# Optimization experiments

Measured on AMD Instinct MI355X. Metric: run time of the kernel, lower is better.

## Reference

```python
import jax, jax.numpy as jnp
import numpy as np

C = 128          # hidden width hard-coded in DirModelToFace
EPS = 1e-5       # BatchNorm1d eps


def sparse_bmm(rows, cols, vals, x, num_rows):
    """Batched sparse @ dense: COO (rows, cols, vals) shared across batch.
    x: [B, K, c] -> [B, num_rows, c]."""
    def one(xb):
        return jax.ops.segment_sum(xb[cols] * vals[:, None], rows, num_segments=num_rows)
    return jax.vmap(one)(x)


def conv1x1_prebn(x, gamma, beta, W, b):
    # GraphConv1x1(batch_norm='pre'): BN (training stats over B*N rows) then Linear
    mean = x.mean((0, 1))
    var = x.var((0, 1))  # biased, as torch BN uses for normalization
    xh = (x - mean) * jax.lax.rsqrt(var + EPS) * gamma + beta
    return xh @ W + b


def dir_block(Di, DiA, v, f, g, be, W, b):
    # DirResNet2 (res_f=False): quaternionic Dirac message passing
    B, N, _ = v.shape
    Fn = f.shape[1]
    msg_v = sparse_bmm(*DiA, f.reshape(B, 4 * Fn, C // 4), 4 * N).reshape(B, N, C)
    x = jax.nn.elu(jnp.concatenate([v, msg_v], axis=-1))
    v_out = v + conv1x1_prebn(x, g[0], be[0], W[0], b[0])
    msg_f = sparse_bmm(*Di, v_out.reshape(B, 4 * N, C // 4), 4 * Fn).reshape(B, Fn, C)
    x = jax.nn.elu(jnp.concatenate([f, msg_f], axis=-1))
    f_out = conv1x1_prebn(x, g[1], be[1], W[1], b[1])  # no residual on f
    return v_out, f_out


def avg_block(mask, v, g, be, W, b):
    # AvgResNet2: masked global average message
    x = v
    for j in range(2):
        x = jax.nn.elu(x)
        x_avg = (mask * x).sum(1, keepdims=True) / mask.sum(1, keepdims=True)
        x = jnp.concatenate([x, jnp.broadcast_to(x_avg, x.shape)], axis=-1)
        x = conv1x1_prebn(x, g[j], be[j], W[j], b[j])
    return x + v


def setup_inputs() -> dict:
    key = jax.random.key(0)
    ks = jax.random.split(key, 10)
    B, N, Fn = 4, 12000, 24000
    nnz = 48 * Fn  # 3 vertices per face x 4x4 quaternion block
    inputs = jax.random.normal(ks[0], (B, N, 3), jnp.float32)
    mask = jnp.ones((B, N, 1), jnp.float32)
    Di_rows = jax.random.randint(ks[1], (nnz,), 0, 4 * Fn, jnp.int32)
    Di_cols = jax.random.randint(ks[2], (nnz,), 0, 4 * N, jnp.int32)
    Di_vals = jax.random.normal(ks[3], (nnz,), jnp.float32) * 0.1
    DiA_rows = jax.random.randint(ks[4], (nnz,), 0, 4 * N, jnp.int32)
    DiA_cols = jax.random.randint(ks[5], (nnz,), 0, 4 * Fn, jnp.int32)
    DiA_vals = jax.random.normal(ks[6], (nnz,), jnp.float32) * 0.1
    W1 = jax.random.normal(ks[7], (3, C), jnp.float32) / np.sqrt(3.0)
    b1 = jnp.zeros((C,), jnp.float32)
    rn_gamma = jnp.ones((16, 2, 2 * C), jnp.float32)
    rn_beta = jnp.zeros((16, 2, 2 * C), jnp.float32)
    rn_W = jax.random.normal(ks[8], (16, 2, 2 * C, C), jnp.float32) / np.sqrt(2.0 * C)
    rn_b = jnp.zeros((16, 2, C), jnp.float32)
    g2 = jnp.ones((C,), jnp.float32)
    be2 = jnp.zeros((C,), jnp.float32)
    W2 = jax.random.normal(ks[9], (C, 1), jnp.float32) / np.sqrt(1.0 * C)
    b2 = jnp.zeros((1,), jnp.float32)
    return dict(inputs=inputs, mask=mask,
                Di_rows=Di_rows, Di_cols=Di_cols, Di_vals=Di_vals,
                DiA_rows=DiA_rows, DiA_cols=DiA_cols, DiA_vals=DiA_vals,
                W1=W1, b1=b1, rn_gamma=rn_gamma, rn_beta=rn_beta, rn_W=rn_W, rn_b=rn_b,
                g2=g2, be2=be2, W2=W2, b2=b2, num_faces=24000)


def reference(inputs, mask, Di_rows, Di_cols, Di_vals, DiA_rows, DiA_cols, DiA_vals,
              W1, b1, rn_gamma, rn_beta, rn_W, rn_b, g2, be2, W2, b2, num_faces):
    B, N, _ = inputs.shape
    v = inputs @ W1 + b1                       # conv1 (batch_norm=None)
    f = jnp.zeros((B, num_faces, C), v.dtype)  # face features start at zero
    Di = (Di_rows, Di_cols, Di_vals)
    DiA = (DiA_rows, DiA_cols, DiA_vals)
    for i in range(16):
        if i % 2 == 0:
            v, f = dir_block(Di, DiA, v, f, rn_gamma[i], rn_beta[i], rn_W[i], rn_b[i])
        else:
            v = avg_block(mask, v, rn_gamma[i], rn_beta[i], rn_W[i], rn_b[i])
    x = jax.nn.elu(f)
    return conv1x1_prebn(x, g2, be2, W2, b2)   # conv2 (batch_norm='pre')
```

## Files before the change

### kernel.cpp

```cpp
#include <hip/hip_runtime.h>
#include <hip/hip_fp16.h>
#include <math.h>


#define EPS 1e-5f

typedef float floatx4 __attribute__((ext_vector_type(4)));
typedef short shortx8 __attribute__((ext_vector_type(8)));

__device__ __forceinline__ float eluf(float x) { return x > 0.f ? x : expm1f(x); }
__device__ __forceinline__ float4 elu4(float4 v) {
    v.x = eluf(v.x); v.y = eluf(v.y); v.z = eluf(v.z); v.w = eluf(v.w); return v;
}
__device__ __forceinline__ short f2bf(float x) {
    unsigned u = __builtin_bit_cast(unsigned, x);
    u = u + 0x7FFFu + ((u >> 16) & 1u);
    return (short)(u >> 16);
}
__device__ __forceinline__ float bf2f(short h) {
    unsigned u = ((unsigned)(unsigned short)h) << 16;
    return __builtin_bit_cast(float, u);
}

__global__ void conv1_kernel(const float* __restrict__ in, const float* __restrict__ W1,
                             const float* __restrict__ b1, float* __restrict__ v,
                             __half* __restrict__ vH, int N, float* __restrict__ Sout) {
    int t = threadIdx.x;
    int c = t & 127, half = t >> 7;
    int r0 = blockIdx.x * 64;
    float w0 = W1[c], w1 = W1[128 + c], w2 = W1[256 + c], bb = b1[c];
    float s1 = 0.f, s2 = 0.f;
    for (int k = 0; k < 32; ++k) {
        int r = r0 + half + 2 * k;
        float x0 = in[r * 3 + 0], x1 = in[r * 3 + 1], x2 = in[r * 3 + 2];
        float val = bb + x0 * w0 + x1 * w1 + x2 * w2;
        v[(size_t)r * 128 + c] = val;
        int b = r / N, vert = r - b * N;
        vH[(size_t)(4 * vert + (c >> 5)) * 128 + b * 32 + (c & 31)] = __float2half(val);
        float e = eluf(val);
        s1 += e; s2 += e * e;
    }
    atomicAdd(&Sout[c], s1);
    atomicAdd(&Sout[256 + c], s2);
}


__global__ void hist_kernel(const int* __restrict__ rows, int* __restrict__ counts) {
    int e = blockIdx.x * 256 + threadIdx.x;
    atomicAdd(&counts[rows[e]], 1);
}

__global__ void partial_kernel(const int* __restrict__ counts, int* __restrict__ partials,
                               int R) {
    int t = threadIdx.x;
    int base = blockIdx.x * 1024 + t * 4;
    int s = 0;
#pragma unroll
    for (int j = 0; j < 4; ++j) { int i = base + j; if (i < R) s += counts[i]; }
    __shared__ int sh[256];
    sh[t] = s; __syncthreads();
    for (int st = 128; st > 0; st >>= 1) {
        if (t < st) sh[t] += sh[t + st];
        __syncthreads();
    }
    if (t == 0) partials[blockIdx.x] = sh[0];
}

__global__ void scanp_kernel(int* __restrict__ partials, int* __restrict__ rowptr,
                             int P, int R, int total) {
    __shared__ int sh[256];
    int t = threadIdx.x;
    int v = (t < P) ? partials[t] : 0;
    sh[t] = v; __syncthreads();
    for (int st = 1; st < 256; st <<= 1) {
        int tmp = (t >= st) ? sh[t - st] : 0;
        __syncthreads();
        sh[t] += tmp;
        __syncthreads();
    }
    if (t < P) partials[t] = sh[t] - v;
    if (t == 0) rowptr[R] = total;
}

__global__ void apply_kernel(int* __restrict__ counts, const int* __restrict__ partials,
                             int* __restrict__ rowptr, int R) {
    int t = threadIdx.x;
    int base = blockIdx.x * 1024 + t * 4;
    int c[4]; int s = 0;
#pragma unroll
    for (int j = 0; j < 4; ++j) { int i = base + j; c[j] = (i < R) ? counts[i] : 0; s += c[j]; }
    __shared__ int sh[256];
    sh[t] = s; __syncthreads();
    for (int st = 1; st < 256; st <<= 1) {
        int tmp = (t >= st) ? sh[t - st] : 0;
        __syncthreads();
        sh[t] += tmp;
        __syncthreads();
    }
    int off = partials[blockIdx.x] + sh[t] - s;
#pragma unroll
    for (int j = 0; j < 4; ++j) {
        int i = base + j;
        if (i < R) { rowptr[i] = off; counts[i] = off; }
        off += c[j];
    }
}

__global__ void scatter_kernel(const int* __restrict__ rows, const int* __restrict__ cols,
                               const float* __restrict__ vals, int* __restrict__ fill,
                               int2* __restrict__ edges) {
    int e = blockIdx.x * 256 + threadIdx.x;
    int p = atomicAdd(&fill[rows[e]], 1);
    edges[p] = make_int2(cols[e], __float_as_int(vals[e]));
}

__global__ __launch_bounds__(1024) void spmm_csr_kernel(
    const int* __restrict__ rowptr, const int2* __restrict__ edges,
    const __half2* __restrict__ xH, float* __restrict__ y, int R4,
    float* __restrict__ Sout) {
    int t = threadIdx.x;
    int waveId = blockIdx.x * 16 + (t >> 6);
    int lane = t & 63;
    int b = lane >> 4, cp = lane & 15;
    const __half2* xb = xH + b * 16 + cp;
    size_t rs = (size_t)R4 * 32;
    __shared__ float red[256];
    if (t < 256) red[t] = 0.f;
    __syncthreads();
#pragma unroll
    for (int rr = 0; rr < 2; ++rr) {
        int r = waveId * 2 + rr;
        int e0 = rowptr[r], e1 = rowptr[r + 1];
        float ax = 0.f, ay = 0.f;
        int e = e0;
        for (; e + 4 <= e1; e += 4) {
            int2 E0 = edges[e], E1 = edges[e + 1], E2 = edges[e + 2], E3 = edges[e + 3];
            __half2 g0 = xb[(size_t)E0.x * 64];
            __half2 g1 = xb[(size_t)E1.x * 64];
            __half2 g2 = xb[(size_t)E2.x * 64];
            __half2 g3 = xb[(size_t)E3.x * 64];
            float v0 = __int_as_float(E0.y), v1 = __int_as_float(E1.y);
            float v2 = __int_as_float(E2.y), v3 = __int_as_float(E3.y);
            float2 f0 = __half22float2(g0), f1 = __half22float2(g1);
            float2 f2 = __half22float2(g2), f3 = __half22float2(g3);
            ax += v0 * f0.x; ay += v0 * f0.y;
            ax += v1 * f1.x; ay += v1 * f1.y;
            ax += v2 * f2.x; ay += v2 * f2.y;
            ax += v3 * f3.x; ay += v3 * f3.y;
        }
        for (; e < e1; ++e) {
            int2 E = edges[e];
            __half2 g = xb[(size_t)E.x * 64];
            float v = __int_as_float(E.y);
            float2 f = __half22float2(g);
            ax += v * f.x; ay += v * f.y;
        }
        *(float2*)&y[(size_t)b * rs + (size_t)r * 32 + cp * 2] = make_float2(ax, ay);
        float ea = eluf(ax), eb = eluf(ay);
        float s1a = ea, s2a = ea * ea, s1b = eb, s2b = eb * eb;
        s1a += __shfl_xor(s1a, 16); s1a += __shfl_xor(s1a, 32);
        s2a += __shfl_xor(s2a, 16); s2a += __shfl_xor(s2a, 32);
        s1b += __shfl_xor(s1b, 16); s1b += __shfl_xor(s1b, 32);
        s2b += __shfl_xor(s2b, 16); s2b += __shfl_xor(s2b, 32);
        if (lane < 16) {
            int ch = (r & 3) * 32 + cp * 2;
            atomicAdd(&red[ch], s1a);
            atomicAdd(&red[ch + 1], s1b);
            atomicAdd(&red[128 + ch], s2a);
            atomicAdd(&red[128 + ch + 1], s2b);
        }
    }
    __syncthreads();
    if (t < 128) atomicAdd(&Sout[128 + t], red[t]);
    else if (t < 256) atomicAdd(&Sout[384 + (t - 128)], red[t]);
}

__global__ void fold_kernel(const float* __restrict__ S, const float* __restrict__ gamma,
                            const float* __restrict__ beta, const float* __restrict__ W,
                            const float* __restrict__ bvec, short* __restrict__ Wh,
                            short* __restrict__ Wl, float* __restrict__ bp, float invR) {
    __shared__ float red[256];
    int o = blockIdx.x, k = threadIdx.x;
    float mean = S[k] * invR;
    float var = S[256 + k] * invR - mean * mean;
    float s = gamma[k] / sqrtf(var + EPS);
    float w = W[(size_t)k * 128 + o];
    float wp = s * w;
    short h = f2bf(wp);
    Wh[(size_t)o * 256 + k] = h;
    Wl[(size_t)o * 256 + k] = f2bf(wp - bf2f(h));
    red[k] = (beta[k] - mean * s) * w;
    __syncthreads();
    for (int st = 128; st > 0; st >>= 1) {
        if (k < st) red[k] += red[k + st];
        __syncthreads();
    }
    if (k == 0) bp[o] = bvec[o] + red[0];
}

__global__ __launch_bounds__(256) void gemm_mfma(
    const float* __restrict__ A, const float* __restrict__ Bs,
    const short* __restrict__ Wh, const short* __restrict__ Wl,
    const float* __restrict__ bp, const float* __restrict__ resid,
    float* __restrict__ out, __half* __restrict__ shadow,
    float* __restrict__ Sout, int rowsPerBatch, int modeB, int eluB) {
    __shared__ short Bsh[128 * 40];
    __shared__ short Bsl[128 * 40];
    const int t = threadIdx.x;
    const int lane = t & 63;
    const int wave = t >> 6;
    const int rowBase = blockIdx.x * 128 + wave * 32;
    const int m = lane & 15;
    const int kq = lane >> 4;
    floatx4 acc[2][8];
#pragma unroll
    for (int i = 0; i < 2; ++i)
#pragma unroll
        for (int j = 0; j < 8; ++j) acc[i][j] = {0.f, 0.f, 0.f, 0.f};

    for (int kb = 0; kb < 8; ++kb) {
        const int k0 = kb * 32 + kq * 8;
        __syncthreads();
#pragma unroll
        for (int i = 0; i < 2; ++i) {
            int idx = t + 256 * i;
            int col = idx >> 2, q = idx & 3;
            shortx8 h = *(const shortx8*)&Wh[(size_t)col * 256 + kb * 32 + q * 8];
            shortx8 l = *(const shortx8*)&Wl[(size_t)col * 256 + kb * 32 + q * 8];
            *(shortx8*)&Bsh[col * 40 + q * 8] = h;
            *(shortx8*)&Bsl[col * 40 + q * 8] = l;
        }
        shortx8 ah[2], al[2];
#pragma unroll
        for (int rg = 0; rg < 2; ++rg) {
            int row = rowBase + rg * 16 + m;
            float4 p, q;
            if (kb < 4) {
                p = elu4(*(const float4*)&A[(size_t)row * 128 + k0]);
                q = elu4(*(const float4*)&A[(size_t)row * 128 + k0 + 4]);
            } else {
                int kk = k0 - 128;
                if (modeB == 0) {
                    p = *(const float4*)&Bs[(size_t)row * 128 + kk];
                    q = *(const float4*)&Bs[(size_t)row * 128 + kk + 4];
                    if (eluB) { p = elu4(p); q = elu4(q); }
                } else {
                    int b = row / rowsPerBatch;
                    p = *(const float4*)&Bs[b * 128 + kk];
                    q = *(const float4*)&Bs[b * 128 + kk + 4];
                }
            }
            float x[8] = {p.x, p.y, p.z, p.w, q.x, q.y, q.z, q.w};
#pragma unroll
            for (int j = 0; j < 8; ++j) {
                short h = f2bf(x[j]);
                ah[rg][j] = h;
                al[rg][j] = f2bf(x[j] - bf2f(h));
            }
        }
        __syncthreads();
#pragma unroll
        for (int ct = 0; ct < 8; ++ct) {
            int co = (ct * 16 + m) * 40 + kq * 8;
            shortx8 bh = *(const shortx8*)&Bsh[co];
            shortx8 bl = *(const shortx8*)&Bsl[co];
#pragma unroll
            for (int rg = 0; rg < 2; ++rg) {
                acc[rg][ct] = __builtin_amdgcn_mfma_f32_16x16x32_bf16(ah[rg], bh, acc[rg][ct], 0, 0, 0);
                acc[rg][ct] = __builtin_amdgcn_mfma_f32_16x16x32_bf16(ah[rg], bl, acc[rg][ct], 0, 0, 0);
                acc[rg][ct] = __builtin_amdgcn_mfma_f32_16x16x32_bf16(al[rg], bh, acc[rg][ct], 0, 0, 0);
            }
        }
    }
    float cs1[8], cs2[8];
#pragma unroll
    for (int ct = 0; ct < 8; ++ct) { cs1[ct] = 0.f; cs2[ct] = 0.f; }
#pragma unroll
    for (int ct = 0; ct < 8; ++ct) {
        int col = ct * 16 + m;
        float bb = bp[col];
#pragma unroll
        for (int rg = 0; rg < 2; ++rg) {
#pragma unroll
            for (int r = 0; r < 4; ++r) {
                int row = rowBase + rg * 16 + kq * 4 + r;
                size_t o = (size_t)row * 128 + col;
                float v = acc[rg][ct][r] + bb;
                if (resid) v += resid[o];
                out[o] = v;
                if (shadow) {
                    int b = row / rowsPerBatch, vert = row - b * rowsPerBatch;
                    shadow[(size_t)(4 * vert + (col >> 5)) * 128 + b * 32 + (col & 31)] =
                        __float2half(v);
                }
                float e = eluf(v);
                cs1[ct] += e; cs2[ct] += e * e;
            }
        }
    }
    if (Sout) {
        __syncthreads();
        float* red = (float*)Bsh;
        red[t] = 0.f;
        __syncthreads();
#pragma unroll
        for (int ct = 0; ct < 8; ++ct) {
            cs1[ct] += __shfl_xor(cs1[ct], 16); cs1[ct] += __shfl_xor(cs1[ct], 32);
            cs2[ct] += __shfl_xor(cs2[ct], 16); cs2[ct] += __shfl_xor(cs2[ct], 32);
        }
        if (kq == 0) {
#pragma unroll
            for (int ct = 0; ct < 8; ++ct) {
                atomicAdd(&red[ct * 16 + m], cs1[ct]);
                atomicAdd(&red[128 + ct * 16 + m], cs2[ct]);
            }
        }
        __syncthreads();
        if (t < 128) atomicAdd(&Sout[t], red[t]);
        else atomicAdd(&Sout[256 + (t - 128)], red[t]);
    }
}

__global__ void avgpool_kernel(const float* __restrict__ X, const float* __restrict__ mask,
                               float* __restrict__ avgacc, float* __restrict__ masksum,
                               int N, int rpb) {
    int b = blockIdx.y, t = threadIdx.x;
    int n0 = blockIdx.x * rpb;
    int n1 = min(n0 + rpb, N);
    float acc = 0.f, mac = 0.f;
    for (int n = n0; n < n1; ++n) {
        float m = mask[(size_t)b * N + n];
        float v = eluf(X[((size_t)b * N + n) * 128 + t]);
        acc += m * v;
        mac += m;
    }
    atomicAdd(&avgacc[b * 128 + t], acc);
    if (t == 0) atomicAdd(&masksum[b], mac);
}

__global__ void finalize_avg(const float* __restrict__ avgacc, const float* __restrict__ masksum,
                             float* __restrict__ avg, float* __restrict__ S, float fN) {
    int c = threadIdx.x;
    float s1 = 0.f, s2 = 0.f;
    for (int b = 0; b < 4; ++b) {
        float a = avgacc[b * 128 + c] / masksum[b];
        avg[b * 128 + c] = a;
        s1 += a; s2 += a * a;
    }
    S[128 + c] = s1 * fN;
    S[256 + 128 + c] = s2 * fN;
}

__global__ void fold_final(const float* __restrict__ S, const float* __restrict__ g2,
                           const float* __restrict__ be2, const float* __restrict__ W2,
                           const float* __restrict__ b2, float* __restrict__ W2p, float invR) {
    __shared__ float red[128];
    int c = threadIdx.x;
    float mean = S[c] * invR;
    float var = S[256 + c] * invR - mean * mean;
    float s = g2[c] / sqrtf(var + EPS);
    float w = W2[c];
    W2p[c] = s * w;
    red[c] = (be2[c] - mean * s) * w;
    __syncthreads();
    for (int st = 64; st > 0; st >>= 1) {
        if (c < st) red[c] += red[c + st];
        __syncthreads();
    }
    if (c == 0) W2p[128] = b2[0] + red[0];
}

__global__ void final_out_kernel(const float* __restrict__ f, const float* __restrict__ W2p,
                                 float* __restrict__ out) {
    int t = threadIdx.x;
    int w = t >> 6, lane = t & 63;
    int row = blockIdx.x * 4 + w;
    float a = eluf(f[(size_t)row * 128 + lane]) * W2p[lane] +
              eluf(f[(size_t)row * 128 + 64 + lane]) * W2p[64 + lane];
    for (int off = 32; off > 0; off >>= 1) a += __shfl_down(a, off);
    if (lane == 0) out[row] = a + W2p[128];
}

extern "C" void kernel_launch(void* const* d_in, const int* in_sizes, int n_in,
                              void* d_out, int out_size, void* d_ws, size_t ws_size,
                              hipStream_t stream) {
    const float* inputs = (const float*)d_in[0];
    const float* mask = (const float*)d_in[1];
    const int* Di_rows = (const int*)d_in[2];
    const int* Di_cols = (const int*)d_in[3];
    const float* Di_vals = (const float*)d_in[4];
    const int* DiA_rows = (const int*)d_in[5];
    const int* DiA_cols = (const int*)d_in[6];
    const float* DiA_vals = (const float*)d_in[7];
    const float* W1 = (const float*)d_in[8];
    const float* b1 = (const float*)d_in[9];
    const float* rn_gamma = (const float*)d_in[10];
    const float* rn_beta = (const float*)d_in[11];
    const float* rn_W = (const float*)d_in[12];
    const float* rn_b = (const float*)d_in[13];
    const float* g2 = (const float*)d_in[14];
    const float* be2 = (const float*)d_in[15];
    const float* W2 = (const float*)d_in[16];
    const float* b2 = (const float*)d_in[17];
    float* out = (float*)d_out;

    const int B = 4;
    const int BN = in_sizes[1];
    const int N = BN / B;
    const int BF = out_size;
    const int Fn = BF / B;
    const int nnz = in_sizes[2];
    const int RA = 4 * N;
    const int RD = 4 * Fn;

    float* ws = (float*)d_ws;
    size_t off = 0;
    float* vA = ws + off;  off += (size_t)BN * 128;
    float* fA = ws + off;  off += (size_t)BF * 128;
    float* msg = ws + off; off += (size_t)BF * 128;
    __half* vH = (__half*)(ws + off); off += (size_t)RA * 128 / 2;
    __half* fH = (__half*)(ws + off); off += (size_t)RD * 128 / 2;
    int* ptrA    = (int*)(ws + off);  off += (size_t)RA + 4;
    int2* edgesA = (int2*)(ws + off); off += (size_t)nnz * 2;
    int* ptrD    = (int*)(ws + off);  off += (size_t)RD + 4;
    int2* edgesD = (int2*)(ws + off); off += (size_t)nnz * 2;
    int* tmpfill = (int*)(ws + off);  off += (size_t)RD;
    int* partials = (int*)(ws + off); off += 256;
    float* Sarena = ws + off; off += 33 * 512;
    float* Aarena = ws + off; off += 16 * 516;
    float* avg = ws + off;    off += 512;
    short* Wh = (short*)(ws + off); off += 128 * 256 / 2;
    short* Wl = (short*)(ws + off); off += 128 * 256 / 2;
    float* bp = ws + off;  off += 128;
    float* W2p = ws + off; off += 132;

    const int eBlocks = nnz / 256;
    const int PA = (RA + 1023) / 1024;
    const int PD = (RD + 1023) / 1024;

    hipMemsetAsync(Sarena, 0, (33 * 512 + 16 * 516) * 4, stream);
    hipMemsetAsync(fA, 0, (size_t)BF * 128 * 4, stream);
    hipMemsetAsync(fH, 0, (size_t)RD * 128 * 2, stream);

    hipMemsetAsync(tmpfill, 0, (size_t)RA * 4, stream);
    hist_kernel<<<eBlocks, 256, 0, stream>>>(DiA_rows, tmpfill);
    partial_kernel<<<PA, 256, 0, stream>>>(tmpfill, partials, RA);
    scanp_kernel<<<1, 256, 0, stream>>>(partials, ptrA, PA, RA, nnz);
    apply_kernel<<<PA, 256, 0, stream>>>(tmpfill, partials, ptrA, RA);
    scatter_kernel<<<eBlocks, 256, 0, stream>>>(DiA_rows, DiA_cols, DiA_vals, tmpfill, edgesA);
    hipMemsetAsync(tmpfill, 0, (size_t)RD * 4, stream);
    hist_kernel<<<eBlocks, 256, 0, stream>>>(Di_rows, tmpfill);
    partial_kernel<<<PD, 256, 0, stream>>>(tmpfill, partials, RD);
    scanp_kernel<<<1, 256, 0, stream>>>(partials, ptrD, PD, RD, nnz);
    apply_kernel<<<PD, 256, 0, stream>>>(tmpfill, partials, ptrD, RD);
    scatter_kernel<<<eBlocks, 256, 0, stream>>>(Di_rows, Di_cols, Di_vals, tmpfill, edgesD);

    auto slot = [&](int i, int j) { return Sarena + 512 * (2 * i + j); };
    float* Sfinal = Sarena + 512 * 32;

    conv1_kernel<<<BN / 64, 256, 0, stream>>>(inputs, W1, b1, vA, vH, N, slot(0, 0));

    int aslot = 0;
    for (int i = 0; i < 15; ++i) {
        if ((i & 1) == 0) {
            const float* g0 = rn_gamma + (size_t)(i * 2 + 0) * 256;
            const float* be0 = rn_beta + (size_t)(i * 2 + 0) * 256;
            const float* Wl0 = rn_W + (size_t)(i * 2 + 0) * 256 * 128;
            const float* bl0 = rn_b + (size_t)(i * 2 + 0) * 128;
            const float* g1 = rn_gamma + (size_t)(i * 2 + 1) * 256;
            const float* be1 = rn_beta + (size_t)(i * 2 + 1) * 256;
            const float* Wl1 = rn_W + (size_t)(i * 2 + 1) * 256 * 128;
            const float* bl1 = rn_b + (size_t)(i * 2 + 1) * 128;

            spmm_csr_kernel<<<RA / 32, 1024, 0, stream>>>(ptrA, edgesA, (const __half2*)fH,
                                                          msg, RA, slot(i, 0));
            fold_kernel<<<128, 256, 0, stream>>>(slot(i, 0), g0, be0, Wl0, bl0, Wh, Wl,
                                                 bp, 1.f / BN);
            gemm_mfma<<<BN / 128, 256, 0, stream>>>(vA, msg, Wh, Wl, bp, vA, vA, vH,
                                                    (i < 14) ? slot(i + 1, 0) : nullptr,
                                                    N, 0, 1);

            spmm_csr_kernel<<<RD / 32, 1024, 0, stream>>>(ptrD, edgesD, (const __half2*)vH,
                                                          msg, RD, slot(i, 1));
            fold_kernel<<<128, 256, 0, stream>>>(slot(i, 1), g1, be1, Wl1, bl1, Wh, Wl,
                                                 bp, 1.f / BF);
            gemm_mfma<<<BF / 128, 256, 0, stream>>>(fA, msg, Wh, Wl, bp, nullptr, fA, fH,
                                                    (i < 14) ? slot(i + 2, 1) : Sfinal,
                                                    Fn, 0, 1);
        } else {
            for (int j = 0; j < 2; ++j) {
                const float* g = rn_gamma + (size_t)(i * 2 + j) * 256;
                const float* be = rn_beta + (size_t)(i * 2 + j) * 256;
                const float* Wlw = rn_W + (size_t)(i * 2 + j) * 256 * 128;
                const float* bl = rn_b + (size_t)(i * 2 + j) * 128;
                const float* src = (j == 0) ? vA : msg;
                float* dst = (j == 0) ? msg : vA;
                const float* resid = (j == 0) ? nullptr : vA;
                __half* shadow = (j == 0) ? nullptr : vH;
                float* Sout = (j == 0) ? slot(i, 1) : slot(i + 1, 0);

                float* avgacc = Aarena + 516 * aslot;
                float* masksum = avgacc + 512;
                aslot++;
                avgpool_kernel<<<dim3(N / 50, B), 128, 0, stream>>>(src, mask, avgacc,
                                                                    masksum, N, 50);
                finalize_avg<<<1, 128, 0, stream>>>(avgacc, masksum, avg, slot(i, j),
                                                    (float)N);
                fold_kernel<<<128, 256, 0, stream>>>(slot(i, j), g, be, Wlw, bl, Wh, Wl,
                                                     bp, 1.f / BN);
                gemm_mfma<<<BN / 128, 256, 0, stream>>>(src, avg, Wh, Wl, bp, resid, dst,
                                                        shadow, Sout, N, 1, 0);
            }
        }
    }

    fold_final<<<1, 128, 0, stream>>>(Sfinal, g2, be2, W2, b2, W2p, 1.f / BF);
    final_out_kernel<<<BF / 4, 256, 0, stream>>>(fA, W2p, out);
}
```

Measured before the change: 4.724 ms.

## Fuse masked average pooling into GEMM epilogue and skip zero face-message work

```diff
diff --git a/kernel.cpp b/kernel.cpp
--- a/kernel.cpp
+++ b/kernel.cpp
@@ -20,6 +20,12 @@
 __device__ __forceinline__ float bf2f(short h) {
     unsigned u = ((unsigned)(unsigned short)h) << 16;
     return __builtin_bit_cast(float, u);
+}
+__device__ __forceinline__ void split2(float x, short& hi, short& lo) {
+    unsigned u = __builtin_bit_cast(unsigned, x);
+    hi = (short)(u >> 16);
+    float r = x - bf2f(hi);
+    lo = (short)(__builtin_bit_cast(unsigned, r) >> 16);
 }
 
 __global__ void conv1_kernel(const float* __restrict__ in, const float* __restrict__ W1,
@@ -42,6 +48,18 @@
     }
     atomicAdd(&Sout[c], s1);
     atomicAdd(&Sout[256 + c], s2);
+}
+
+__global__ void masksum_kernel(const float* __restrict__ mask, float* __restrict__ msum,
+                               int N) {
+    int b = blockIdx.x, t = threadIdx.x;
+    float s = 0.f;
+    for (int n = t; n < N; n += 256) s += mask[(size_t)b * N + n];
+    for (int o = 32; o > 0; o >>= 1) s += __shfl_down(s, o);
+    __shared__ float sh[4];
+    if ((t & 63) == 0) sh[t >> 6] = s;
+    __syncthreads();
+    if (t == 0) msum[b] = sh[0] + sh[1] + sh[2] + sh[3];
 }
 
 
@@ -203,7 +221,8 @@
     const short* __restrict__ Wh, const short* __restrict__ Wl,
     const float* __restrict__ bp, const float* __restrict__ resid,
     float* __restrict__ out, __half* __restrict__ shadow,
-    float* __restrict__ Sout, int rowsPerBatch, int modeB, int eluB) {
+    float* __restrict__ Sout, const float* __restrict__ mask,
+    float* __restrict__ avgout, int rowsPerBatch, int modeB, int eluB) {
     __shared__ short Bsh[128 * 40];
     __shared__ short Bsl[128 * 40];
     const int t = threadIdx.x;
@@ -218,7 +237,8 @@
 #pragma unroll
         for (int j = 0; j < 8; ++j) acc[i][j] = {0.f, 0.f, 0.f, 0.f};
 
-    for (int kb = 0; kb < 8; ++kb) {
+    const int kbEnd = (modeB == 2) ? 4 : 8;
+    for (int kb = 0; kb < kbEnd; ++kb) {
         const int k0 = kb * 32 + kq * 8;
         __syncthreads();
 #pragma unroll
@@ -253,9 +273,10 @@
             float x[8] = {p.x, p.y, p.z, p.w, q.x, q.y, q.z, q.w};
 #pragma unroll
             for (int j = 0; j < 8; ++j) {
-                short h = f2bf(x[j]);
+                short h, l;
+                split2(x[j], h, l);
                 ah[rg][j] = h;
-                al[rg][j] = f2bf(x[j] - bf2f(h));
+                al[rg][j] = l;
             }
         }
         __syncthreads();
@@ -272,9 +293,21 @@
             }
         }
     }
-    float cs1[8], cs2[8];
-#pragma unroll
-    for (int ct = 0; ct < 8; ++ct) { cs1[ct] = 0.f; cs2[ct] = 0.f; }
+    const int bBlk = (blockIdx.x * 128) / rowsPerBatch;
+    float mk8[8]; int ib8[8];
+    if (avgout) {
+#pragma unroll
+        for (int rg = 0; rg < 2; ++rg)
+#pragma unroll
+            for (int r = 0; r < 4; ++r) {
+                int row = rowBase + rg * 16 + kq * 4 + r;
+                mk8[rg * 4 + r] = mask[row];
+                ib8[rg * 4 + r] = (row >= (bBlk + 1) * rowsPerBatch) ? 1 : 0;
+            }
+    }
+    float cs1[8], cs2[8], av0[8], av1[8];
+#pragma unroll
+    for (int ct = 0; ct < 8; ++ct) { cs1[ct] = 0.f; cs2[ct] = 0.f; av0[ct] = 0.f; av1[ct] = 0.f; }
 #pragma unroll
     for (int ct = 0; ct < 8; ++ct) {
         int col = ct * 16 + m;
@@ -295,47 +328,49 @@
                 }
                 float e = eluf(v);
                 cs1[ct] += e; cs2[ct] += e * e;
+                if (avgout) {
+                    float me = mk8[rg * 4 + r] * e;
+                    if (ib8[rg * 4 + r]) av1[ct] += me; else av0[ct] += me;
+                }
             }
         }
     }
     if (Sout) {
         __syncthreads();
         float* red = (float*)Bsh;
+        float* redv = (float*)Bsl;
         red[t] = 0.f;
+        if (avgout) redv[t] = 0.f;
         __syncthreads();
 #pragma unroll
         for (int ct = 0; ct < 8; ++ct) {
             cs1[ct] += __shfl_xor(cs1[ct], 16); cs1[ct] += __shfl_xor(cs1[ct], 32);
             cs2[ct] += __shfl_xor(cs2[ct], 16); cs2[ct] += __shfl_xor(cs2[ct], 32);
+            if (avgout) {
+                av0[ct] += __shfl_xor(av0[ct], 16); av0[ct] += __shfl_xor(av0[ct], 32);
+                av1[ct] += __shfl_xor(av1[ct], 16); av1[ct] += __shfl_xor(av1[ct], 32);
+            }
         }
         if (kq == 0) {
 #pragma unroll
             for (int ct = 0; ct < 8; ++ct) {
                 atomicAdd(&red[ct * 16 + m], cs1[ct]);
                 atomicAdd(&red[128 + ct * 16 + m], cs2[ct]);
+                if (avgout) {
+                    atomicAdd(&redv[ct * 16 + m], av0[ct]);
+                    atomicAdd(&redv[128 + ct * 16 + m], av1[ct]);
+                }
             }
         }
         __syncthreads();
         if (t < 128) atomicAdd(&Sout[t], red[t]);
         else atomicAdd(&Sout[256 + (t - 128)], red[t]);
-    }
-}
-
-__global__ void avgpool_kernel(const float* __restrict__ X, const float* __restrict__ mask,
-                               float* __restrict__ avgacc, float* __restrict__ masksum,
-                               int N, int rpb) {
-    int b = blockIdx.y, t = threadIdx.x;
-    int n0 = blockIdx.x * rpb;
-    int n1 = min(n0 + rpb, N);
-    float acc = 0.f, mac = 0.f;
-    for (int n = n0; n < n1; ++n) {
-        float m = mask[(size_t)b * N + n];
-        float v = eluf(X[((size_t)b * N + n) * 128 + t]);
-        acc += m * v;
-        mac += m;
-    }
-    atomicAdd(&avgacc[b * 128 + t], acc);
-    if (t == 0) atomicAdd(&masksum[b], mac);
+        if (avgout) {
+            int plane = t >> 7, col = t & 127;
+            int b = bBlk + plane;
+            if (b < 4) atomicAdd(&avgout[b * 128 + col], redv[t]);
+        }
+    }
 }
 
 __global__ void finalize_avg(const float* __restrict__ avgacc, const float* __restrict__ masksum,
@@ -427,7 +462,8 @@
     int* tmpfill = (int*)(ws + off);  off += (size_t)RD;
     int* partials = (int*)(ws + off); off += 256;
     float* Sarena = ws + off; off += 33 * 512;
-    float* Aarena = ws + off; off += 16 * 516;
+    float* Aarena = ws + off; off += 16 * 512;
+    float* msum = ws + off;   off += 4;
     float* avg = ws + off;    off += 512;
     short* Wh = (short*)(ws + off); off += 128 * 256 / 2;
     short* Wl = (short*)(ws + off); off += 128 * 256 / 2;
@@ -438,9 +474,8 @@
     const int PA = (RA + 1023) / 1024;
     const int PD = (RD + 1023) / 1024;
 
-    hipMemsetAsync(Sarena, 0, (33 * 512 + 16 * 516) * 4, stream);
+    hipMemsetAsync(Sarena, 0, (33 * 512 + 16 * 512) * 4, stream);
     hipMemsetAsync(fA, 0, (size_t)BF * 128 * 4, stream);
-    hipMemsetAsync(fH, 0, (size_t)RD * 128 * 2, stream);
 
     hipMemsetAsync(tmpfill, 0, (size_t)RA * 4, stream);
     hist_kernel<<<eBlocks, 256, 0, stream>>>(DiA_rows, tmpfill);
@@ -458,9 +493,9 @@
     auto slot = [&](int i, int j) { return Sarena + 512 * (2 * i + j); };
     float* Sfinal = Sarena + 512 * 32;
 
+    masksum_kernel<<<B, 256, 0, stream>>>(mask, msum, N);
     conv1_kernel<<<BN / 64, 256, 0, stream>>>(inputs, W1, b1, vA, vH, N, slot(0, 0));
 
-    int aslot = 0;
     for (int i = 0; i < 15; ++i) {
         if ((i & 1) == 0) {
             const float* g0 = rn_gamma + (size_t)(i * 2 + 0) * 256;
@@ -471,14 +506,23 @@
             const float* be1 = rn_beta + (size_t)(i * 2 + 1) * 256;
             const float* Wl1 = rn_W + (size_t)(i * 2 + 1) * 256 * 128;
             const float* bl1 = rn_b + (size_t)(i * 2 + 1) * 128;
-
-            spmm_csr_kernel<<<RA / 32, 1024, 0, stream>>>(ptrA, edgesA, (const __half2*)fH,
-                                                          msg, RA, slot(i, 0));
-            fold_kernel<<<128, 256, 0, stream>>>(slot(i, 0), g0, be0, Wl0, bl0, Wh, Wl,
-                                                 bp, 1.f / BN);
-            gemm_mfma<<<BN / 128, 256, 0, stream>>>(vA, msg, Wh, Wl, bp, vA, vA, vH,
-                                                    (i < 14) ? slot(i + 1, 0) : nullptr,
-                                                    N, 0, 1);
+            float* SoutV = (i < 14) ? slot(i + 1, 0) : nullptr;
+            float* avgV = (i < 14) ? (Aarena + 512 * i) : nullptr;
+
+            if (i == 0) {
+                fold_kernel<<<128, 256, 0, stream>>>(slot(0, 0), g0, be0, Wl0, bl0,
+                                                     Wh, Wl, bp, 1.f / BN);
+                gemm_mfma<<<BN / 128, 256, 0, stream>>>(vA, nullptr, Wh, Wl, bp, vA, vA,
+                                                        vH, SoutV, mask, avgV, N, 2, 1);
+            } else {
+                spmm_csr_kernel<<<RA / 32, 1024, 0, stream>>>(ptrA, edgesA,
+                                                              (const __half2*)fH, msg, RA,
+                                                              slot(i, 0));
+                fold_kernel<<<128, 256, 0, stream>>>(slot(i, 0), g0, be0, Wl0, bl0,
+                                                     Wh, Wl, bp, 1.f / BN);
+                gemm_mfma<<<BN / 128, 256, 0, stream>>>(vA, msg, Wh, Wl, bp, vA, vA,
+                                                        vH, SoutV, mask, avgV, N, 0, 1);
+            }
 
             spmm_csr_kernel<<<RD / 32, 1024, 0, stream>>>(ptrD, edgesD, (const __half2*)vH,
                                                           msg, RD, slot(i, 1));
@@ -486,7 +530,7 @@
                                                  bp, 1.f / BF);
             gemm_mfma<<<BF / 128, 256, 0, stream>>>(fA, msg, Wh, Wl, bp, nullptr, fA, fH,
                                                     (i < 14) ? slot(i + 2, 1) : Sfinal,
-                                                    Fn, 0, 1);
+                                                    nullptr, nullptr, Fn, 0, 1);
         } else {
             for (int j = 0; j < 2; ++j) {
                 const float* g = rn_gamma + (size_t)(i * 2 + j) * 256;
@@ -498,18 +542,15 @@
                 const float* resid = (j == 0) ? nullptr : vA;
                 __half* shadow = (j == 0) ? nullptr : vH;
                 float* Sout = (j == 0) ? slot(i, 1) : slot(i + 1, 0);
-
-                float* avgacc = Aarena + 516 * aslot;
-                float* masksum = avgacc + 512;
-                aslot++;
-                avgpool_kernel<<<dim3(N / 50, B), 128, 0, stream>>>(src, mask, avgacc,
-                                                                    masksum, N, 50);
-                finalize_avg<<<1, 128, 0, stream>>>(avgacc, masksum, avg, slot(i, j),
+                float* avgO = (j == 0) ? (Aarena + 512 * i) : nullptr;
+
+                float* avgacc = Aarena + 512 * (i - 1 + j);
+                finalize_avg<<<1, 128, 0, stream>>>(avgacc, msum, avg, slot(i, j),
                                                     (float)N);
                 fold_kernel<<<128, 256, 0, stream>>>(slot(i, j), g, be, Wlw, bl, Wh, Wl,
                                                      bp, 1.f / BN);
                 gemm_mfma<<<BN / 128, 256, 0, stream>>>(src, avg, Wh, Wl, bp, resid, dst,
-                                                        shadow, Sout, N, 1, 0);
+                                                        shadow, Sout, mask, avgO, N, 1, 0);
             }
         }
     }
```

Result: faster. 4.195 ms (-11.2%).
